# Optimization experiments

Hardware: AMD Instinct MI355X
Metric: run time of the kernel (lower is better)

The kernel has to match this reference:

```python
import jax, jax.numpy as jnp
import numpy as np

N, D, K = 262144, 256, 640
BETA = 0.25
# Faithful to original including the start = end + 1 off-by-one between partitions.
STARTS = jnp.array([0, 129, 257, 385, 513, 577], dtype=jnp.int32)
ENDS = jnp.array([128, 256, 384, 512, 576, 640], dtype=jnp.int32)


def setup_inputs() -> dict:
    key = jax.random.key(0)
    k1, k2, k3 = jax.random.split(key, 3)
    x = jax.random.randint(k1, (N, 2), 0, 121, dtype=jnp.int64)
    e = jax.random.normal(k2, (N, D), dtype=jnp.float32)
    weights = jax.random.normal(k3, (K, D), dtype=jnp.float32)
    return {"x": x, "e": e, "weights": weights}


def _partition_id(atom_type):
    # order: C(5)->0, N(6)->1, O(7)->2, others->3, mask119->4, mask120->5
    pid = jnp.full(atom_type.shape, 3, dtype=jnp.int32)
    pid = jnp.where(atom_type == 5, 0, pid)
    pid = jnp.where(atom_type == 6, 1, pid)
    pid = jnp.where(atom_type == 7, 2, pid)
    pid = jnp.where(atom_type == 119, 4, pid)
    pid = jnp.where(atom_type == 120, 5, pid)
    return pid


def reference(x, e, weights):
    atom_type = x[:, 0]
    pid = _partition_id(atom_type)                      # (n,)
    start = STARTS[pid]                                 # (n,)
    end = ENDS[pid]                                     # (n,)
    # squared euclidean distances to all 640 codes: (n, K)
    d2 = (jnp.sum(e * e, axis=1, keepdims=True)
          + jnp.sum(weights * weights, axis=1)[None, :]
          - 2.0 * (e @ weights.T))
    codes = jnp.arange(K, dtype=jnp.int32)
    mask = (codes[None, :] >= start[:, None]) & (codes[None, :] < end[:, None])
    idx = jnp.argmin(jnp.where(mask, d2, jnp.inf), axis=1)  # absolute code index
    quantized = weights[idx]                            # (n, d)
    codebook_loss = jnp.mean((quantized - jax.lax.stop_gradient(e)) ** 2)
    gnn_loss = jnp.mean((e - jax.lax.stop_gradient(quantized)) ** 2)
    vq_loss = codebook_loss + BETA * gnn_loss
    out = e + jax.lax.stop_gradient(quantized - e)      # straight-through
    return out, codebook_loss, gnn_loss, vq_loss
```

## Files before the change

kernel.cpp:

```cpp
#include <hip/hip_runtime.h>
#include <cstdint>
#include <cstddef>

#define N_ROWS 262144
#define D 256
#define K_CODES 640
#define BM 64
#define BK 32
#define TAU 0.05f

typedef __attribute__((ext_vector_type(8))) short bf16x8;
typedef __attribute__((ext_vector_type(4))) float f32x4;

__constant__ int d_STARTS[6] = {0, 129, 257, 385, 513, 577};
__constant__ int d_ENDS[6]   = {128, 256, 384, 512, 576, 640};

__device__ __forceinline__ int partition_id(int a) {
    int p = 3;
    if (a == 5) p = 0;
    else if (a == 6) p = 1;
    else if (a == 7) p = 2;
    else if (a == 119) p = 4;
    else if (a == 120) p = 5;
    return p;
}

__device__ __forceinline__ unsigned short f32_to_bf16_rne(float x) {
    unsigned int u = __float_as_uint(x);
    u += 0x7FFFu + ((u >> 16) & 1u);
    return (unsigned short)(u >> 16);
}


__global__ void k_zero(int* ws_i) {
    int t = threadIdx.x;
    for (int i = t; i < 2048; i += 256) ws_i[i] = 0;
}

__global__ void k_wnorm(const float* __restrict__ w, double* __restrict__ wnorm2,
                        float* __restrict__ wnormf) {
    int k = blockIdx.x;
    int l = threadIdx.x;
    const float* row = w + (size_t)k * D;
    double s = 0.0;
    for (int j = l; j < D; j += 64) {
        double v = (double)row[j];
        s += v * v;
    }
    #pragma unroll
    for (int m = 32; m > 0; m >>= 1) s += __shfl_xor(s, m, 64);
    if (l == 0) { wnorm2[k] = s; wnormf[k] = (float)s; }
}

__global__ void k_wfrag(const float* __restrict__ w, unsigned short* __restrict__ wfrag) {
    int blk = blockIdx.x;
    int p = blk >> 3, kt = blk & 7;
    int cs = d_STARTS[p], ce = d_ENDS[p];
    int t = threadIdx.x;
    #pragma unroll
    for (int i = 0; i < 4; i++) {
        int s = i * 256 + t;
        int h = s >> 9;
        int ct = (s >> 6) & 7;
        int lane = s & 63;
        int k = cs + 16 * ct + (lane & 15);
        int c0 = kt * 32 + 8 * (lane >> 4);
        unsigned v0 = 0, v1 = 0, v2 = 0, v3 = 0;
        if (k < ce) {
            const float* row = w + (size_t)k * D + c0;
            unsigned vv[4];
            #pragma unroll
            for (int j = 0; j < 4; j++) {
                float x0 = row[2 * j], x1 = row[2 * j + 1];
                unsigned short a0 = f32_to_bf16_rne(x0), a1 = f32_to_bf16_rne(x1);
                if (h) {
                    float y0 = x0 - __uint_as_float((unsigned)a0 << 16);
                    float y1 = x1 - __uint_as_float((unsigned)a1 << 16);
                    a0 = f32_to_bf16_rne(y0);
                    a1 = f32_to_bf16_rne(y1);
                }
                vv[j] = (unsigned)a0 | ((unsigned)a1 << 16);
            }
            v0 = vv[0]; v1 = vv[1]; v2 = vv[2]; v3 = vv[3];
        }
        *(uint4*)(wfrag + ((size_t)blk * 1024 + s) * 8) = make_uint4(v0, v1, v2, v3);
    }
}

__global__ void k_count(const int* __restrict__ x, int* __restrict__ counts) {
    __shared__ int lc[6];
    int t = threadIdx.x;
    if (t < 6) lc[t] = 0;
    __syncthreads();
    int r = blockIdx.x * 1024 + t;
    atomicAdd(&lc[partition_id(x[2 * r])], 1);
    __syncthreads();
    if (t < 6) atomicAdd(&counts[t], lc[t]);
}

__global__ void k_scan(const int* __restrict__ counts, int* __restrict__ bases,
                       int* __restrict__ cursors) {
    if (threadIdx.x == 0) {
        int b = 0;
        for (int p = 0; p < 6; p++) {
            bases[p] = b;
            cursors[p] = b;
            b += counts[p];
        }
    }
}

__global__ void k_scatter(const int* __restrict__ x, int* __restrict__ cursors,
                          int* __restrict__ rowlist) {
    __shared__ int wcnt[16][6];
    __shared__ int bbase[6];
    int t = threadIdx.x;
    int wid = t >> 6, lane = t & 63;
    int r = blockIdx.x * 1024 + t;
    int p = partition_id(x[2 * r]);
    unsigned long long mym = 0;
    #pragma unroll
    for (int q = 0; q < 6; q++) {
        unsigned long long m = __ballot(p == q);
        if (p == q) mym = m;
        if (lane == 0) wcnt[wid][q] = __popcll(m);
    }
    __syncthreads();
    if (t < 6) {
        int s = 0;
        for (int w2 = 0; w2 < 16; w2++) { int c = wcnt[w2][t]; wcnt[w2][t] = s; s += c; }
        bbase[t] = atomicAdd(&cursors[t], s);
    }
    __syncthreads();
    int pos = bbase[p] + wcnt[wid][p] + __popcll(mym & ((1ull << lane) - 1ull));
    rowlist[pos] = r;
}

__launch_bounds__(256, 5)
__global__ void k_passA(const float* __restrict__ e, const float* __restrict__ w,
                        const int* __restrict__ counts, const int* __restrict__ bases,
                        const int* __restrict__ rowlist, const unsigned short* __restrict__ wfrag,
                        const float* __restrict__ wnormf,
                        float* __restrict__ out, double* __restrict__ loss,
                        int* __restrict__ flagcnt, int* __restrict__ flagrows) {
    int b = blockIdx.x;
    int p = -1, seg = 0;
    {
        int acc0 = 0;
        for (int q = 0; q < 6; q++) {
            int nb = (counts[q] + BM - 1) / BM;
            if (b < acc0 + nb) { p = q; seg = b - acc0; break; }
            acc0 += nb;
        }
    }
    if (p < 0) return;

    int cstart = d_STARTS[p], cend = d_ENDS[p];
    int cnt = counts[p];
    int base = bases[p] + seg * BM;
    int nrows = min(BM, cnt - seg * BM);

    __shared__ int rl[BM];
    __shared__ float wnf[128];
    __shared__ int bestk[BM];
    __shared__ double lred[4];
    __shared__ __align__(16) unsigned short Ah[4][64][8];
    __shared__ __align__(16) unsigned short Al[4][64][8];
    __shared__ __align__(16) unsigned short Bf[2][8][64][8];

    int tid = threadIdx.x;
    int lane = tid & 63;
    int wid = tid >> 6;
    int m16 = lane & 15;

    if (tid < BM) rl[tid] = (tid < nrows) ? rowlist[base + tid] : -1;
    if (tid < 128) {
        int k = cstart + tid;
        wnf[tid] = (k < cend) ? wnormf[k] : __int_as_float(0x7f800000);
    }
    __syncthreads();

    f32x4 acc[8];
    #pragma unroll
    for (int ct = 0; ct < 8; ct++) acc[ct] = (f32x4){0.f, 0.f, 0.f, 0.f};

    double lsum = 0.0;

    int srow = tid >> 2;
    int q4 = tid & 3;
    int gr = rl[srow];
    const float* ebase = e + (size_t)(gr < 0 ? 0 : gr) * D + 8 * q4;
    unsigned short* aw_h = &Ah[srow >> 4][(srow & 15) + 16 * q4][0];
    unsigned short* aw_l = &Al[srow >> 4][(srow & 15) + 16 * q4][0];
    const unsigned short* wtile = wfrag + (size_t)p * 8 * 8192;
    unsigned short* bbuf = &Bf[0][0][0][0];

    #pragma unroll 1
    for (int t0 = 0; t0 < D; t0 += BK) {
        {
            const unsigned short* wt = wtile + (size_t)(t0 >> 5) * 8192;
            #pragma unroll
            for (int i = 0; i < 4; i++) {
                int ws_ = i * 256 + wid * 64;
                __builtin_amdgcn_global_load_lds(
                    (const __attribute__((address_space(1))) unsigned int*)(wt + (size_t)(ws_ + lane) * 8),
                    (__attribute__((address_space(3))) unsigned int*)(bbuf + (size_t)ws_ * 8),
                    16, 0, 0);
            }
        }
        {
            float4 ev0 = make_float4(0.f, 0.f, 0.f, 0.f);
            float4 ev1 = make_float4(0.f, 0.f, 0.f, 0.f);
            if (gr >= 0) {
                ev0 = *(const float4*)(ebase + t0);
                ev1 = *(const float4*)(ebase + t0 + 4);
            }
            float n0 = ev0.x * ev0.x + ev0.y * ev0.y + ev0.z * ev0.z + ev0.w * ev0.w;
            float n1 = ev1.x * ev1.x + ev1.y * ev1.y + ev1.z * ev1.z + ev1.w * ev1.w;
            lsum += (double)(n0 + n1);
            unsigned short h0 = f32_to_bf16_rne(ev0.x), h1 = f32_to_bf16_rne(ev0.y);
            unsigned short h2 = f32_to_bf16_rne(ev0.z), h3 = f32_to_bf16_rne(ev0.w);
            unsigned short h4 = f32_to_bf16_rne(ev1.x), h5 = f32_to_bf16_rne(ev1.y);
            unsigned short h6 = f32_to_bf16_rne(ev1.z), h7 = f32_to_bf16_rne(ev1.w);
            float r0 = ev0.x - __uint_as_float((unsigned)h0 << 16);
            float r1 = ev0.y - __uint_as_float((unsigned)h1 << 16);
            float r2 = ev0.z - __uint_as_float((unsigned)h2 << 16);
            float r3 = ev0.w - __uint_as_float((unsigned)h3 << 16);
            float r4 = ev1.x - __uint_as_float((unsigned)h4 << 16);
            float r5 = ev1.y - __uint_as_float((unsigned)h5 << 16);
            float r6 = ev1.z - __uint_as_float((unsigned)h6 << 16);
            float r7 = ev1.w - __uint_as_float((unsigned)h7 << 16);
            uint4 hp = make_uint4((unsigned)h0 | ((unsigned)h1 << 16),
                                  (unsigned)h2 | ((unsigned)h3 << 16),
                                  (unsigned)h4 | ((unsigned)h5 << 16),
                                  (unsigned)h6 | ((unsigned)h7 << 16));
            uint4 lp = make_uint4((unsigned)f32_to_bf16_rne(r0) | ((unsigned)f32_to_bf16_rne(r1) << 16),
                                  (unsigned)f32_to_bf16_rne(r2) | ((unsigned)f32_to_bf16_rne(r3) << 16),
                                  (unsigned)f32_to_bf16_rne(r4) | ((unsigned)f32_to_bf16_rne(r5) << 16),
                                  (unsigned)f32_to_bf16_rne(r6) | ((unsigned)f32_to_bf16_rne(r7) << 16));
            *(uint4*)aw_h = hp;
            *(uint4*)aw_l = lp;
        }
        __syncthreads();

        bf16x8 a_h = *(const bf16x8*)&Ah[wid][lane][0];
        bf16x8 a_l = *(const bf16x8*)&Al[wid][lane][0];
        #pragma unroll
        for (int ct = 0; ct < 8; ct++) {
            bf16x8 b_h = *(const bf16x8*)&Bf[0][ct][lane][0];
            bf16x8 b_l = *(const bf16x8*)&Bf[1][ct][lane][0];
            acc[ct] = __builtin_amdgcn_mfma_f32_16x16x32_bf16(a_h, b_h, acc[ct], 0, 0, 0);
            acc[ct] = __builtin_amdgcn_mfma_f32_16x16x32_bf16(a_l, b_h, acc[ct], 0, 0, 0);
            acc[ct] = __builtin_amdgcn_mfma_f32_16x16x32_bf16(a_h, b_l, acc[ct], 0, 0, 0);
        }
        __syncthreads();
    }

    float wl[8];
    #pragma unroll
    for (int ct = 0; ct < 8; ct++) wl[ct] = wnf[16 * ct + m16];

    const float INFF = __int_as_float(0x7f800000);
    #pragma unroll
    for (int reg = 0; reg < 4; reg++) {
        int slot = 16 * wid + (lane >> 4) * 4 + reg;
        float b1 = INFF, b2 = INFF;
        int c1 = 1 << 30, c2 = 1 << 30;
        #pragma unroll
        for (int ct = 0; ct < 8; ct++) {
            float s = wl[ct] - 2.0f * acc[ct][reg];
            int k = cstart + 16 * ct + m16;
            if (s < b1) { b2 = b1; c2 = c1; b1 = s; c1 = k; }
            else if (s < b2) { b2 = s; c2 = k; }
        }
        #pragma unroll
        for (int m = 1; m < 16; m <<= 1) {
            float ob1 = __shfl_xor(b1, m, 64), ob2 = __shfl_xor(b2, m, 64);
            int oc1 = __shfl_xor(c1, m, 64), oc2 = __shfl_xor(c2, m, 64);
            bool oWins = (ob1 < b1) || (ob1 == b1 && oc1 < c1);
            if (oWins) {
                float nb2; int nc2;
                if (b1 < ob2 || (b1 == ob2 && c1 < oc2)) { nb2 = b1; nc2 = c1; }
                else { nb2 = ob2; nc2 = oc2; }
                b1 = ob1; c1 = oc1; b2 = nb2; c2 = nc2;
            } else {
                if (ob1 < b2 || (ob1 == b2 && oc1 < c2)) { b2 = ob1; c2 = oc1; }
            }
        }
        if (m16 == 0) {
            if (slot < nrows) {
                if (b2 - b1 < TAU) {
                    int pos = atomicAdd(flagcnt, 1);
                    flagrows[pos] = rl[slot];
                    bestk[slot] = -1;
                } else {
                    bestk[slot] = c1;
                    lsum += (double)b1;
                }
            } else {
                bestk[slot] = -1;
            }
        }
    }
    __syncthreads();

    for (int rsl = wid; rsl < nrows; rsl += 4) {
        int k = bestk[rsl];
        if (k >= 0) {
            int g = rl[rsl];
            *(float4*)(out + (size_t)g * D + 4 * lane) =
                *(const float4*)(w + (size_t)k * D + 4 * lane);
        }
    }

    #pragma unroll
    for (int m = 32; m > 0; m >>= 1) lsum += __shfl_xor(lsum, m, 64);
    if (lane == 0) lred[wid] = lsum;
    __syncthreads();
    if (tid == 0) atomicAdd(loss, lred[0] + lred[1] + lred[2] + lred[3]);
}

__global__ void k_passB(const float* __restrict__ e, const float* __restrict__ w,
                        const int* __restrict__ x, const double* __restrict__ wnorm2,
                        const int* __restrict__ flagcnt, const int* __restrict__ flagrows,
                        float* __restrict__ out, double* __restrict__ loss) {
    __shared__ float eL[D];
    __shared__ double sc[128];
    __shared__ int sk[128];
    int t = threadIdx.x;
    int nf = *flagcnt;
    for (int f = blockIdx.x; f < nf; f += gridDim.x) {
        int gr = flagrows[f];
        eL[t] = e[(size_t)gr * D + t];
        __syncthreads();
        int p = partition_id(x[2 * gr]);
        int cs = d_STARTS[p], ce = d_ENDS[p];
        if (t < 128) {
            int k = cs + t;
            if (k < ce) {
                const float* wr = w + (size_t)k * D;
                double d0 = 0.0, d1 = 0.0, d2 = 0.0, d3 = 0.0;
                #pragma unroll 4
                for (int d = 0; d < D; d += 4) {
                    d0 += (double)eL[d + 0] * (double)wr[d + 0];
                    d1 += (double)eL[d + 1] * (double)wr[d + 1];
                    d2 += (double)eL[d + 2] * (double)wr[d + 2];
                    d3 += (double)eL[d + 3] * (double)wr[d + 3];
                }
                sc[t] = wnorm2[k] - 2.0 * ((d0 + d1) + (d2 + d3));
                sk[t] = k;
            } else {
                sc[t] = 1e300;
                sk[t] = 1 << 30;
            }
        }
        __syncthreads();
        for (int s = 64; s > 0; s >>= 1) {
            if (t < s) {
                double o = sc[t + s]; int ok = sk[t + s];
                if (o < sc[t] || (o == sc[t] && ok < sk[t])) { sc[t] = o; sk[t] = ok; }
            }
            __syncthreads();
        }
        int bk = sk[0];
        out[(size_t)gr * D + t] = w[(size_t)bk * D + t];
        if (t == 0) atomicAdd(loss, sc[0]);
        __syncthreads();
    }
}

__global__ void k_final(const double* __restrict__ loss, float* __restrict__ out) {
    if (threadIdx.x == 0) {
        double mean = *loss / ((double)N_ROWS * (double)D);
        size_t nd = (size_t)N_ROWS * D;
        out[nd + 0] = (float)mean;
        out[nd + 1] = (float)mean;
        out[nd + 2] = (float)(1.25 * mean);
    }
}

extern "C" void kernel_launch(void* const* d_in, const int* in_sizes, int n_in,
                              void* d_out, int out_size, void* d_ws, size_t ws_size,
                              hipStream_t stream) {
    const int* x = (const int*)d_in[0];
    const float* e = (const float*)d_in[1];
    const float* w = (const float*)d_in[2];
    float* out = (float*)d_out;
    char* ws = (char*)d_ws;

    double* loss    = (double*)(ws + 0);
    double* wnorm2  = (double*)(ws + 8);
    int* counts     = (int*)(ws + 5128);
    int* bases      = (int*)(ws + 5152);
    int* cursors    = (int*)(ws + 5176);
    int* flagcnt    = (int*)(ws + 5200);
    float* wnormf   = (float*)(ws + 5208);
    int* rowlist    = (int*)(ws + 8192);
    int* flagrows   = (int*)(ws + 8192 + 4 * (size_t)N_ROWS);
    unsigned short* wfrag = (unsigned short*)(ws + 8192 + 8 * (size_t)N_ROWS);

    k_zero<<<1, 256, 0, stream>>>((int*)ws);
    k_wnorm<<<K_CODES, 64, 0, stream>>>(w, wnorm2, wnormf);
    k_wfrag<<<48, 256, 0, stream>>>(w, wfrag);
    k_count<<<N_ROWS / 1024, 1024, 0, stream>>>(x, counts);
    k_scan<<<1, 64, 0, stream>>>(counts, bases, cursors);
    k_scatter<<<N_ROWS / 1024, 1024, 0, stream>>>(x, cursors, rowlist);
    k_passA<<<N_ROWS / BM + 5, 256, 0, stream>>>(e, w, counts, bases, rowlist, wfrag,
                                                 wnormf, out, loss, flagcnt, flagrows);
    k_passB<<<512, 256, 0, stream>>>(e, w, x, wnorm2, flagcnt, flagrows, out, loss);
    k_final<<<1, 64, 0, stream>>>(loss, out);
}
```

Baseline: 525.2 us.

## Load A fragments directly into registers and prefetch next e tile

Each lane now loads its own row slice of e straight into the MFMA A-operand layout, so the split bf16 hi/lo fragments never pass through shared memory. The Ah/Al LDS buffers and their write/read round trip go away. The next K-step's e values are also prefetched into registers while the current step computes, and the loop is fully unrolled. This hides global load latency behind MFMA work, at the cost of more VGPRs.

```diff
diff --git a/kernel.cpp b/kernel.cpp
--- a/kernel.cpp
+++ b/kernel.cpp
@@ -164,8 +164,6 @@
     __shared__ float wnf[128];
     __shared__ int bestk[BM];
     __shared__ double lred[4];
-    __shared__ __align__(16) unsigned short Ah[4][64][8];
-    __shared__ __align__(16) unsigned short Al[4][64][8];
     __shared__ __align__(16) unsigned short Bf[2][8][64][8];
 
     int tid = threadIdx.x;
@@ -186,19 +184,23 @@
 
     double lsum = 0.0;
 
-    int srow = tid >> 2;
-    int q4 = tid & 3;
-    int gr = rl[srow];
-    const float* ebase = e + (size_t)(gr < 0 ? 0 : gr) * D + 8 * q4;
-    unsigned short* aw_h = &Ah[srow >> 4][(srow & 15) + 16 * q4][0];
-    unsigned short* aw_l = &Al[srow >> 4][(srow & 15) + 16 * q4][0];
+    int gr = rl[16 * wid + m16];
+    bool valid = gr >= 0;
+    const float* ebase = e + (size_t)(valid ? gr : 0) * D + 8 * (lane >> 4);
     const unsigned short* wtile = wfrag + (size_t)p * 8 * 8192;
     unsigned short* bbuf = &Bf[0][0][0][0];
 
-    #pragma unroll 1
-    for (int t0 = 0; t0 < D; t0 += BK) {
+    const float4 z4 = make_float4(0.f, 0.f, 0.f, 0.f);
+    float4 p0 = z4, p1 = z4;
+    if (valid) {
+        p0 = *(const float4*)(ebase + 0);
+        p1 = *(const float4*)(ebase + 4);
+    }
+
+    #pragma unroll
+    for (int tt = 0; tt < 8; ++tt) {
         {
-            const unsigned short* wt = wtile + (size_t)(t0 >> 5) * 8192;
+            const unsigned short* wt = wtile + (size_t)tt * 8192;
             #pragma unroll
             for (int i = 0; i < 4; i++) {
                 int ws_ = i * 256 + wid * 64;
@@ -208,52 +210,49 @@
                     16, 0, 0);
             }
         }
-        {
-            float4 ev0 = make_float4(0.f, 0.f, 0.f, 0.f);
-            float4 ev1 = make_float4(0.f, 0.f, 0.f, 0.f);
-            if (gr >= 0) {
-                ev0 = *(const float4*)(ebase + t0);
-                ev1 = *(const float4*)(ebase + t0 + 4);
-            }
-            float n0 = ev0.x * ev0.x + ev0.y * ev0.y + ev0.z * ev0.z + ev0.w * ev0.w;
-            float n1 = ev1.x * ev1.x + ev1.y * ev1.y + ev1.z * ev1.z + ev1.w * ev1.w;
-            lsum += (double)(n0 + n1);
-            unsigned short h0 = f32_to_bf16_rne(ev0.x), h1 = f32_to_bf16_rne(ev0.y);
-            unsigned short h2 = f32_to_bf16_rne(ev0.z), h3 = f32_to_bf16_rne(ev0.w);
-            unsigned short h4 = f32_to_bf16_rne(ev1.x), h5 = f32_to_bf16_rne(ev1.y);
-            unsigned short h6 = f32_to_bf16_rne(ev1.z), h7 = f32_to_bf16_rne(ev1.w);
-            float r0 = ev0.x - __uint_as_float((unsigned)h0 << 16);
-            float r1 = ev0.y - __uint_as_float((unsigned)h1 << 16);
-            float r2 = ev0.z - __uint_as_float((unsigned)h2 << 16);
-            float r3 = ev0.w - __uint_as_float((unsigned)h3 << 16);
-            float r4 = ev1.x - __uint_as_float((unsigned)h4 << 16);
-            float r5 = ev1.y - __uint_as_float((unsigned)h5 << 16);
-            float r6 = ev1.z - __uint_as_float((unsigned)h6 << 16);
-            float r7 = ev1.w - __uint_as_float((unsigned)h7 << 16);
-            uint4 hp = make_uint4((unsigned)h0 | ((unsigned)h1 << 16),
-                                  (unsigned)h2 | ((unsigned)h3 << 16),
-                                  (unsigned)h4 | ((unsigned)h5 << 16),
-                                  (unsigned)h6 | ((unsigned)h7 << 16));
-            uint4 lp = make_uint4((unsigned)f32_to_bf16_rne(r0) | ((unsigned)f32_to_bf16_rne(r1) << 16),
-                                  (unsigned)f32_to_bf16_rne(r2) | ((unsigned)f32_to_bf16_rne(r3) << 16),
-                                  (unsigned)f32_to_bf16_rne(r4) | ((unsigned)f32_to_bf16_rne(r5) << 16),
-                                  (unsigned)f32_to_bf16_rne(r6) | ((unsigned)f32_to_bf16_rne(r7) << 16));
-            *(uint4*)aw_h = hp;
-            *(uint4*)aw_l = lp;
-        }
+        float4 n0 = z4, n1 = z4;
+        if (tt < 7 && valid) {
+            n0 = *(const float4*)(ebase + 32 * (tt + 1));
+            n1 = *(const float4*)(ebase + 32 * (tt + 1) + 4);
+        }
+        float n0s = p0.x * p0.x + p0.y * p0.y + p0.z * p0.z + p0.w * p0.w;
+        float n1s = p1.x * p1.x + p1.y * p1.y + p1.z * p1.z + p1.w * p1.w;
+        lsum += (double)(n0s + n1s);
+        unsigned short h0 = f32_to_bf16_rne(p0.x), h1 = f32_to_bf16_rne(p0.y);
+        unsigned short h2 = f32_to_bf16_rne(p0.z), h3 = f32_to_bf16_rne(p0.w);
+        unsigned short h4 = f32_to_bf16_rne(p1.x), h5 = f32_to_bf16_rne(p1.y);
+        unsigned short h6 = f32_to_bf16_rne(p1.z), h7 = f32_to_bf16_rne(p1.w);
+        float r0 = p0.x - __uint_as_float((unsigned)h0 << 16);
+        float r1 = p0.y - __uint_as_float((unsigned)h1 << 16);
+        float r2 = p0.z - __uint_as_float((unsigned)h2 << 16);
+        float r3 = p0.w - __uint_as_float((unsigned)h3 << 16);
+        float r4 = p1.x - __uint_as_float((unsigned)h4 << 16);
+        float r5 = p1.y - __uint_as_float((unsigned)h5 << 16);
+        float r6 = p1.z - __uint_as_float((unsigned)h6 << 16);
+        float r7 = p1.w - __uint_as_float((unsigned)h7 << 16);
+        union { bf16x8 v; uint4 u; } Ah, Al;
+        Ah.u = make_uint4((unsigned)h0 | ((unsigned)h1 << 16),
+                          (unsigned)h2 | ((unsigned)h3 << 16),
+                          (unsigned)h4 | ((unsigned)h5 << 16),
+                          (unsigned)h6 | ((unsigned)h7 << 16));
+        Al.u = make_uint4((unsigned)f32_to_bf16_rne(r0) | ((unsigned)f32_to_bf16_rne(r1) << 16),
+                          (unsigned)f32_to_bf16_rne(r2) | ((unsigned)f32_to_bf16_rne(r3) << 16),
+                          (unsigned)f32_to_bf16_rne(r4) | ((unsigned)f32_to_bf16_rne(r5) << 16),
+                          (unsigned)f32_to_bf16_rne(r6) | ((unsigned)f32_to_bf16_rne(r7) << 16));
+
         __syncthreads();
 
-        bf16x8 a_h = *(const bf16x8*)&Ah[wid][lane][0];
-        bf16x8 a_l = *(const bf16x8*)&Al[wid][lane][0];
         #pragma unroll
         for (int ct = 0; ct < 8; ct++) {
             bf16x8 b_h = *(const bf16x8*)&Bf[0][ct][lane][0];
             bf16x8 b_l = *(const bf16x8*)&Bf[1][ct][lane][0];
-            acc[ct] = __builtin_amdgcn_mfma_f32_16x16x32_bf16(a_h, b_h, acc[ct], 0, 0, 0);
-            acc[ct] = __builtin_amdgcn_mfma_f32_16x16x32_bf16(a_l, b_h, acc[ct], 0, 0, 0);
-            acc[ct] = __builtin_amdgcn_mfma_f32_16x16x32_bf16(a_h, b_l, acc[ct], 0, 0, 0);
+            acc[ct] = __builtin_amdgcn_mfma_f32_16x16x32_bf16(Ah.v, b_h, acc[ct], 0, 0, 0);
+            acc[ct] = __builtin_amdgcn_mfma_f32_16x16x32_bf16(Al.v, b_h, acc[ct], 0, 0, 0);
+            acc[ct] = __builtin_amdgcn_mfma_f32_16x16x32_bf16(Ah.v, b_l, acc[ct], 0, 0, 0);
         }
         __syncthreads();
+
+        p0 = n0; p1 = n1;
     }
 
     float wl[8];
```

New measurement: 611.9 us. +16.5%, slower.
